# Optimization experiments

Hardware: AMD Instinct MI355X
Metric: run time of the kernel (lower is better)

The kernel has to match this reference:

```python
import jax, jax.numpy as jnp
import numpy as np
from jax import lax

B, C, H, W = 16, 512, 32, 32
CQ = C // 16


def _conv(x, w, b):
    # NCHW input, OIHW kernel, 3x3 stride-1 'SAME' == torch padding=1
    o = lax.conv_general_dilated(x, w, (1, 1), 'SAME',
                                 dimension_numbers=('NCHW', 'OIHW', 'NCHW'))
    return o + b[None, :, None, None]


def setup_inputs() -> dict:
    key = jax.random.key(0)
    ks = jax.random.split(key, 8)
    fan_q = C * 9
    fan_v = C * 9
    return {
        'x': jax.random.normal(ks[0], (B, C, H, W), jnp.float32),
        'y': jax.random.normal(ks[1], (B, C, H, W), jnp.float32),
        'wq': jax.random.normal(ks[2], (CQ, C, 3, 3), jnp.float32) / np.sqrt(fan_q),
        'bq': jnp.zeros((CQ,), jnp.float32),
        'wk': jax.random.normal(ks[3], (CQ, C, 3, 3), jnp.float32) / np.sqrt(fan_q),
        'bk': jnp.zeros((CQ,), jnp.float32),
        'wv': jax.random.normal(ks[4], (C, C, 3, 3), jnp.float32) / np.sqrt(fan_v),
        'bv': jnp.zeros((C,), jnp.float32),
    }


def reference(x, y, wq, bq, wk, bk, wv, bv):
    b, c, h, w = x.shape
    n = h * w
    q = _conv(x, wq, bq).reshape(b, -1, n)   # (B, CQ, N)
    k = _conv(y, wk, bk).reshape(b, -1, n)   # (B, CQ, N)
    v = _conv(y, wv, bv).reshape(b, c, n)    # (B, C, N)
    # energy[b, i, j] = <q[:, i], k[:, j]>  (unscaled, non-causal)
    energy = jnp.einsum('bdi,bdj->bij', q, k)           # (B, N, N)
    attn = jax.nn.softmax(energy, axis=-1)              # softmax over keys j
    # out[b, c, i] = sum_j v[b, c, j] * attn[b, i, j]
    out = jnp.einsum('bcj,bij->bci', v, attn)           # (B, C, N)
    return out.reshape(b, c, h, w)
```

## Files before the change

kernel.cpp:

```cpp
#include <hip/hip_runtime.h>

#define BB 16
#define CCH 512
#define CQD 32
#define HH 32
#define WW 32
#define NN 1024

typedef __attribute__((ext_vector_type(8))) _Float16 half8;
typedef __attribute__((ext_vector_type(4))) _Float16 half4;
typedef __attribute__((ext_vector_type(4))) float f32x4;

static __device__ __forceinline__ void gload_lds16(const void* g, void* l) {
    __builtin_amdgcn_global_load_lds(
        (const __attribute__((address_space(1))) unsigned int*)g,
        (__attribute__((address_space(3))) unsigned int*)l, 16, 0, 0);
}

__global__ __launch_bounds__(256) void prep_img_kernel(
    const float* __restrict__ x, const float* __restrict__ y,
    _Float16* __restrict__ xh, _Float16* __restrict__ yh)
{
    const int h = blockIdx.x, which = blockIdx.y, b = blockIdx.z;
    const float* img = which ? y : x;
    _Float16* imgh   = which ? yh : xh;
    __shared__ float X[64][33];
    const int t = threadIdx.x;
    for (int ci0 = 0; ci0 < CCH; ci0 += 64) {
        __syncthreads();
        #pragma unroll
        for (int i = 0; i < 8; ++i) {
            int ci = i * 8 + (t >> 5), w = t & 31;
            X[ci][w] = img[((size_t)(b * CCH + ci0 + ci) * HH + h) * WW + w];
        }
        __syncthreads();
        int w = t >> 3, g = t & 7;
        half8 o;
        #pragma unroll
        for (int u = 0; u < 8; ++u) o[u] = (_Float16)X[g * 8 + u][w];
        *(half8*)&imgh[(((size_t)b * HH + h) * WW + w) * CCH + ci0 + g * 8] = o;
    }
}

__global__ __launch_bounds__(256) void prep_w_all_kernel(
    const float* __restrict__ wv, const float* __restrict__ wq,
    const float* __restrict__ wk, _Float16* __restrict__ wvh,
    _Float16* __restrict__ wqkh)
{
    const int bid = blockIdx.x;
    const float* src;
    _Float16* dst;
    int co_src, co_dst;
    if (bid < 512)      { src = wv; co_src = bid;       dst = wvh;  co_dst = bid; }
    else if (bid < 544) { src = wq; co_src = bid - 512; dst = wqkh; co_dst = bid - 512; }
    else                { src = wk; co_src = bid - 544; dst = wqkh; co_dst = 32 + (bid - 544); }
    for (int idx = threadIdx.x; idx < 4608; idx += 256) {
        int tap = idx / 512, ci = idx - tap * 512;
        dst[(size_t)co_dst * 4608 + idx] = (_Float16)src[(size_t)co_src * 4608 + ci * 9 + tap];
    }
}

__global__ __launch_bounds__(256, 2) void conv_v_mfma_kernel(
    const _Float16* __restrict__ yh,
    const _Float16* __restrict__ wvh,
    const float* __restrict__ bvb,
    _Float16* __restrict__ vout)
{
    const int pt  = blockIdx.x;
    const int co0 = blockIdx.y * 64;
    const int b   = blockIdx.z;

    __shared__ __align__(16) _Float16 Wl[64 * 296];
    __shared__ __align__(16) _Float16 Yl[10 * 34 * 40];

    const int t    = threadIdx.x;
    const int lane = t & 63;
    const int wv4  = t >> 6;
    const int l15  = lane & 15;
    const int kg   = lane >> 4;

    f32x4 acc[4][4];
    #pragma unroll
    for (int m = 0; m < 4; ++m)
        #pragma unroll
        for (int n = 0; n < 4; ++n) {
            f32x4 z = {0.f, 0.f, 0.f, 0.f};
            acc[m][n] = z;
        }

    const int r0 = pt * 8;
    int bbase[4];
    #pragma unroll
    for (int n = 0; n < 4; ++n) {
        int pxl = wv4 * 64 + n * 16 + l15;
        int rl = pxl >> 5, cl = pxl & 31;
        bbase[n] = (rl * 34 + cl) * 40 + kg * 8;
    }
    int abase[4];
    #pragma unroll
    for (int m = 0; m < 4; ++m)
        abase[m] = (m * 16 + l15) * 296 + kg * 8;

    #pragma unroll 1
    for (int ci0 = 0; ci0 < CCH; ci0 += 32) {
        __syncthreads();
        #pragma unroll
        for (int i = 0; i < 10; ++i) {
            int d = t + i * 256;
            if (d < 2368) {
                int c = d / 37, rem = d - c * 37;
                const _Float16* g = (rem < 36)
                    ? &wvh[(size_t)(co0 + c) * 4608 + (rem >> 2) * 512 + ci0 + (rem & 3) * 8]
                    : wvh;
                gload_lds16(g, (char*)Wl + (size_t)(i * 256 + wv4 * 64) * 16);
            }
        }
        for (int idx = t; idx < 1360; idx += 256) {
            int hw = idx >> 2, part = idx & 3;
            int r = hw / 34, c = hw - r * 34;
            int gh = r0 - 1 + r, gw = c - 1;
            half8 v;
            if (gh >= 0 && gh < HH && gw >= 0 && gw < WW) {
                v = *(const half8*)&yh[(((size_t)b * HH + gh) * WW + gw) * CCH + ci0 + part * 8];
            } else {
                #pragma unroll
                for (int u = 0; u < 8; ++u) v[u] = (_Float16)0.f;
            }
            *(half8*)&Yl[(r * 34 + c) * 40 + part * 8] = v;
        }
        __syncthreads();

        #pragma unroll
        for (int tap = 0; tap < 9; ++tap) {
            const int dh = tap / 3, dw = tap % 3;
            half8 a[4], bf[4];
            #pragma unroll
            for (int m = 0; m < 4; ++m)
                a[m] = *(const half8*)&Wl[abase[m] + tap * 32];
            #pragma unroll
            for (int n = 0; n < 4; ++n)
                bf[n] = *(const half8*)&Yl[bbase[n] + (dh * 34 + dw) * 40];
            #pragma unroll
            for (int m = 0; m < 4; ++m)
                #pragma unroll
                for (int n = 0; n < 4; ++n)
                    acc[m][n] = __builtin_amdgcn_mfma_f32_16x16x32_f16(a[m], bf[n], acc[m][n], 0, 0, 0);
        }
    }

    #pragma unroll
    for (int m = 0; m < 4; ++m) {
        #pragma unroll
        for (int reg = 0; reg < 4; ++reg) {
            int co = co0 + m * 16 + kg * 4 + reg;
            float bias = bvb[co];
            #pragma unroll
            for (int n = 0; n < 4; ++n) {
                int px = pt * 256 + wv4 * 64 + n * 16 + l15;
                vout[((size_t)b * CCH + co) * NN + px] = (_Float16)(acc[m][n][reg] + bias);
            }
        }
    }
}

__global__ __launch_bounds__(256, 4) void conv_qk_split_kernel(
    const _Float16* __restrict__ xh,
    const _Float16* __restrict__ yh,
    const _Float16* __restrict__ wqkh,
    float* __restrict__ pbuf)
{
    const int pt    = blockIdx.x >> 2;
    const int ks    = blockIdx.x & 3;
    const int which = blockIdx.y;
    const int b     = blockIdx.z;
    const _Float16* in = which ? yh : xh;

    __shared__ _Float16 Wl[32 * 296];
    __shared__ _Float16 Xl[6 * 34 * 40];

    const int t    = threadIdx.x;
    const int lane = t & 63;
    const int w    = t >> 6;
    const int l15  = lane & 15;
    const int kg   = lane >> 4;

    f32x4 acc[2][2];
    #pragma unroll
    for (int m = 0; m < 2; ++m)
        #pragma unroll
        for (int n = 0; n < 2; ++n) {
            f32x4 z = {0.f, 0.f, 0.f, 0.f};
            acc[m][n] = z;
        }

    const int r0 = pt * 4;
    int bbase[2];
    #pragma unroll
    for (int n = 0; n < 2; ++n) {
        int pxl = w * 32 + n * 16 + l15;
        int rl = pxl >> 5, cl = pxl & 31;
        bbase[n] = (rl * 34 + cl) * 40 + kg * 8;
    }
    int abase[2];
    #pragma unroll
    for (int m = 0; m < 2; ++m)
        abase[m] = (m * 16 + l15) * 296 + kg * 8;

    #pragma unroll 1
    for (int cc = 0; cc < 4; ++cc) {
        const int ci0 = ks * 128 + cc * 32;
        __syncthreads();
        for (int idx = t; idx < 1152; idx += 256) {
            int c = idx / 36, rem = idx - c * 36;
            int tap = rem >> 2, part = rem & 3;
            half8 v = *(const half8*)&wqkh[(size_t)(which * 32 + c) * 4608 + tap * 512 + ci0 + part * 8];
            *(half8*)&Wl[c * 296 + tap * 32 + part * 8] = v;
        }
        for (int idx = t; idx < 816; idx += 256) {
            int hw = idx >> 2, part = idx & 3;
            int r = hw / 34, c = hw - r * 34;
            int gh = r0 - 1 + r, gw = c - 1;
            half8 v;
            if (gh >= 0 && gh < HH && gw >= 0 && gw < WW) {
                v = *(const half8*)&in[(((size_t)b * HH + gh) * WW + gw) * CCH + ci0 + part * 8];
            } else {
                #pragma unroll
                for (int u = 0; u < 8; ++u) v[u] = (_Float16)0.f;
            }
            *(half8*)&Xl[(r * 34 + c) * 40 + part * 8] = v;
        }
        __syncthreads();

        #pragma unroll
        for (int tap = 0; tap < 9; ++tap) {
            const int dh = tap / 3, dw = tap % 3;
            half8 a[2], bfr[2];
            #pragma unroll
            for (int m = 0; m < 2; ++m)
                a[m] = *(const half8*)&Wl[abase[m] + tap * 32];
            #pragma unroll
            for (int n = 0; n < 2; ++n)
                bfr[n] = *(const half8*)&Xl[bbase[n] + (dh * 34 + dw) * 40];
            #pragma unroll
            for (int m = 0; m < 2; ++m)
                #pragma unroll
                for (int n = 0; n < 2; ++n)
                    acc[m][n] = __builtin_amdgcn_mfma_f32_16x16x32_f16(a[m], bfr[n], acc[m][n], 0, 0, 0);
        }
    }

    float* pb = &pbuf[(((size_t)(ks * 2 + which) * BB + b) * NN) * CQD];
    #pragma unroll
    for (int n = 0; n < 2; ++n) {
        int px = pt * 128 + w * 32 + n * 16 + l15;
        #pragma unroll
        for (int m = 0; m < 2; ++m) {
            float4 o = make_float4(acc[m][n][0], acc[m][n][1], acc[m][n][2], acc[m][n][3]);
            *(float4*)&pb[(size_t)px * CQD + m * 16 + kg * 4] = o;
        }
    }
}

__global__ __launch_bounds__(256) void qk_reduce_kernel(
    const float* __restrict__ pbuf,
    const float* __restrict__ bq, const float* __restrict__ bk,
    _Float16* __restrict__ qh, _Float16* __restrict__ kh)
{
    const int gid   = blockIdx.x * 256 + threadIdx.x;
    const int cog   = gid & 7;
    const int px    = (gid >> 3) & 1023;
    const int b     = (gid >> 13) & 15;
    const int which = gid >> 17;

    const size_t base = (((size_t)which * BB + b) * NN + px) * CQD + cog * 4;
    const size_t kstep = (size_t)2 * BB * NN * CQD;
    float4 s = *(const float4*)&pbuf[base];
    #pragma unroll
    for (int ks = 1; ks < 4; ++ks) {
        float4 p = *(const float4*)&pbuf[base + ks * kstep];
        s.x += p.x; s.y += p.y; s.z += p.z; s.w += p.w;
    }
    const float* bias = which ? bk : bq;
    float4 bv = *(const float4*)&bias[cog * 4];
    half4 o;
    o[0] = (_Float16)(s.x + bv.x);
    o[1] = (_Float16)(s.y + bv.y);
    o[2] = (_Float16)(s.z + bv.z);
    o[3] = (_Float16)(s.w + bv.w);
    _Float16* out = which ? kh : qh;
    *(half4*)&out[((size_t)b * NN + px) * CQD + cog * 4] = o;
}

__global__ __launch_bounds__(256, 2) void attn_fused_kernel(
    const _Float16* __restrict__ qh,
    const _Float16* __restrict__ kh,
    const _Float16* __restrict__ v,
    float* __restrict__ out)
{
    const int wg   = blockIdx.x;
    const int virt = (wg & 7) * 64 + (wg >> 3);
    const int b    = virt >> 5;
    const int i0   = (virt & 31) * 32;

    __shared__ _Float16 Kl[128 * 40];
    __shared__ _Float16 Vl[128 * 136];
    __shared__ _Float16 Pl[32 * 136];
    __shared__ float redm[32][17];
    __shared__ float redl[32][17];

    const int t    = threadIdx.x;
    const int lane = t & 63;
    const int w    = t >> 6;
    const int l15  = lane & 15;
    const int kg   = lane >> 4;

    half8 qb[2];
    #pragma unroll
    for (int n = 0; n < 2; ++n)
        qb[n] = *(const half8*)&qh[((size_t)b * NN + i0 + n * 16 + l15) * CQD + kg * 8];

    float m[2] = {-3.0e38f, -3.0e38f}, l[2] = {0.f, 0.f};
    #pragma unroll 1
    for (int jp = 0; jp < 8; ++jp) {
        __syncthreads();
        #pragma unroll
        for (int r = 0; r < 2; ++r) {
            int idx = t + r * 256;
            int j = idx >> 2, part = idx & 3;
            *(half8*)&Kl[j * 40 + part * 8] =
                *(const half8*)&kh[((size_t)b * NN + jp * 128 + j) * CQD + part * 8];
        }
        __syncthreads();
        #pragma unroll
        for (int ht = 0; ht < 2; ++ht) {
            half8 ak = *(const half8*)&Kl[(ht * 64 + w * 16 + l15) * 40 + kg * 8];
            #pragma unroll
            for (int n = 0; n < 2; ++n) {
                f32x4 s = {0.f, 0.f, 0.f, 0.f};
                s = __builtin_amdgcn_mfma_f32_16x16x32_f16(ak, qb[n], s, 0, 0, 0);
                float tm = fmaxf(fmaxf(s[0], s[1]), fmaxf(s[2], s[3]));
                float m2 = fmaxf(m[n], tm);
                l[n] = l[n] * __expf(m[n] - m2)
                     + __expf(s[0] - m2) + __expf(s[1] - m2)
                     + __expf(s[2] - m2) + __expf(s[3] - m2);
                m[n] = m2;
            }
        }
    }
    __syncthreads();
    #pragma unroll
    for (int n = 0; n < 2; ++n) {
        redm[n * 16 + l15][w * 4 + kg] = m[n];
        redl[n * 16 + l15][w * 4 + kg] = l[n];
    }
    __syncthreads();
    float mr[2], rl[2];
    #pragma unroll
    for (int n = 0; n < 2; ++n) {
        const int i = n * 16 + l15;
        float M = redm[i][0];
        #pragma unroll
        for (int p = 1; p < 16; ++p) M = fmaxf(M, redm[i][p]);
        float L = 0.f;
        #pragma unroll
        for (int p = 0; p < 16; ++p) L += redl[i][p] * __expf(redm[i][p] - M);
        mr[n] = M;
        rl[n] = 1.f / L;
    }

    f32x4 acc[4][2][2];
    #pragma unroll
    for (int cc = 0; cc < 4; ++cc)
        #pragma unroll
        for (int mm = 0; mm < 2; ++mm)
            #pragma unroll
            for (int n = 0; n < 2; ++n) {
                f32x4 z = {0.f, 0.f, 0.f, 0.f};
                acc[cc][mm][n] = z;
            }

    #pragma unroll 1
    for (int jp = 0; jp < 8; ++jp) {
        __syncthreads();
        #pragma unroll
        for (int r = 0; r < 2; ++r) {
            int idx = t + r * 256;
            int j = idx >> 2, part = idx & 3;
            *(half8*)&Kl[j * 40 + part * 8] =
                *(const half8*)&kh[((size_t)b * NN + jp * 128 + j) * CQD + part * 8];
        }
        __syncthreads();
        #pragma unroll
        for (int ht = 0; ht < 2; ++ht) {
            half8 ak = *(const half8*)&Kl[(ht * 64 + w * 16 + l15) * 40 + kg * 8];
            #pragma unroll
            for (int n = 0; n < 2; ++n) {
                f32x4 s = {0.f, 0.f, 0.f, 0.f};
                s = __builtin_amdgcn_mfma_f32_16x16x32_f16(ak, qb[n], s, 0, 0, 0);
                half4 p4;
                #pragma unroll
                for (int reg = 0; reg < 4; ++reg)
                    p4[reg] = (_Float16)(__expf(s[reg] - mr[n]) * rl[n]);
                *(half4*)&Pl[(n * 16 + l15) * 136 + ht * 64 + w * 16 + kg * 4] = p4;
            }
        }
        #pragma unroll
        for (int cc = 0; cc < 4; ++cc) {
            __syncthreads();
            #pragma unroll
            for (int r = 0; r < 8; ++r) {
                int idx = t + r * 256;
                int c = idx >> 4, part = idx & 15;
                *(half8*)&Vl[c * 136 + part * 8] =
                    *(const half8*)&v[((size_t)b * CCH + cc * 128 + c) * NN + jp * 128 + part * 8];
            }
            __syncthreads();
            #pragma unroll
            for (int ks = 0; ks < 4; ++ks) {
                half8 pb[2], va[2];
                #pragma unroll
                for (int n = 0; n < 2; ++n)
                    pb[n] = *(const half8*)&Pl[(n * 16 + l15) * 136 + ks * 32 + kg * 8];
                #pragma unroll
                for (int mm = 0; mm < 2; ++mm)
                    va[mm] = *(const half8*)&Vl[(w * 32 + mm * 16 + l15) * 136 + ks * 32 + kg * 8];
                #pragma unroll
                for (int mm = 0; mm < 2; ++mm)
                    #pragma unroll
                    for (int n = 0; n < 2; ++n)
                        acc[cc][mm][n] = __builtin_amdgcn_mfma_f32_16x16x32_f16(va[mm], pb[n], acc[cc][mm][n], 0, 0, 0);
            }
        }
    }

    #pragma unroll
    for (int cc = 0; cc < 4; ++cc)
        #pragma unroll
        for (int mm = 0; mm < 2; ++mm)
            #pragma unroll
            for (int n = 0; n < 2; ++n)
                #pragma unroll
                for (int reg = 0; reg < 4; ++reg) {
                    int c = cc * 128 + w * 32 + mm * 16 + kg * 4 + reg;
                    out[((size_t)b * CCH + c) * NN + i0 + n * 16 + l15] = acc[cc][mm][n][reg];
                }
}

extern "C" void kernel_launch(void* const* d_in, const int* in_sizes, int n_in,
                              void* d_out, int out_size, void* d_ws, size_t ws_size,
                              hipStream_t stream) {
    const float* x  = (const float*)d_in[0];
    const float* y  = (const float*)d_in[1];
    const float* wq = (const float*)d_in[2];
    const float* bq = (const float*)d_in[3];
    const float* wk = (const float*)d_in[4];
    const float* bk = (const float*)d_in[5];
    const float* wv = (const float*)d_in[6];
    const float* bv = (const float*)d_in[7];
    float* out = (float*)d_out;

    _Float16* qhb = (_Float16*)d_ws;
    _Float16* khb = qhb + (size_t)BB * NN * CQD;
    _Float16* vb   = khb + (size_t)BB * NN * CQD;
    _Float16* yhb  = vb + (size_t)BB * CCH * NN;
    _Float16* xhb  = yhb + (size_t)BB * NN * CCH;
    _Float16* wvh  = xhb + (size_t)BB * NN * CCH;
    _Float16* wqkh = wvh + (size_t)512 * 4608;
    float* pbuf = (float*)vb;

    prep_img_kernel<<<dim3(HH, 2, BB), 256, 0, stream>>>(x, y, xhb, yhb);
    prep_w_all_kernel<<<dim3(576), 256, 0, stream>>>(wv, wq, wk, wvh, wqkh);
    conv_qk_split_kernel<<<dim3(32, 2, BB), 256, 0, stream>>>(xhb, yhb, wqkh, pbuf);
    qk_reduce_kernel<<<dim3(1024), 256, 0, stream>>>(pbuf, bq, bk, qhb, khb);
    conv_v_mfma_kernel<<<dim3(4, 8, BB), 256, 0, stream>>>(yhb, wvh, bv, vb);
    attn_fused_kernel<<<dim3(512), 256, 0, stream>>>(qhb, khb, vb, out);
}
```

Baseline: 181.8 us.

## Pre-pad fp16 images and use direct global-to-LDS loads in conv kernels

The image prep kernel now writes zero-padded 34x34 NHWC fp16 buffers, so the convolution tile loads need no bounds checks. Both the V conv and the QK conv replace register-staged LDS fills with global_load_lds 16-byte async copies, using a 5-slot row stride (40 halves) that matches the existing padded LDS layout. The QK weight tile also switches to direct LDS loads. This removes per-element branching and VGPR round trips in the load phase, at the cost of slightly larger workspace buffers and extra padding writes in the prep kernel.

```diff
diff --git a/kernel.cpp b/kernel.cpp
--- a/kernel.cpp
+++ b/kernel.cpp
@@ -6,6 +6,7 @@
 #define HH 32
 #define WW 32
 #define NN 1024
+#define PH 34
 
 typedef __attribute__((ext_vector_type(8))) _Float16 half8;
 typedef __attribute__((ext_vector_type(4))) _Float16 half4;
@@ -19,26 +20,43 @@
 
 __global__ __launch_bounds__(256) void prep_img_kernel(
     const float* __restrict__ x, const float* __restrict__ y,
-    _Float16* __restrict__ xh, _Float16* __restrict__ yh)
+    _Float16* __restrict__ xp, _Float16* __restrict__ yp)
 {
-    const int h = blockIdx.x, which = blockIdx.y, b = blockIdx.z;
+    const int h = blockIdx.x;
+    const int which = blockIdx.y, b = blockIdx.z;
     const float* img = which ? y : x;
-    _Float16* imgh   = which ? yh : xh;
+    _Float16* row = (which ? yp : xp) + (size_t)(b * PH + h) * PH * CCH;
+    const int t = threadIdx.x;
+    const int gh = h - 1;
+
+    half8 z;
+    #pragma unroll
+    for (int u = 0; u < 8; ++u) z[u] = (_Float16)0.f;
+
+    if (gh < 0 || gh >= HH) {
+        for (int idx = t; idx < PH * CCH / 8; idx += 256)
+            *(half8*)&row[(size_t)idx * 8] = z;
+        return;
+    }
+
     __shared__ float X[64][33];
-    const int t = threadIdx.x;
     for (int ci0 = 0; ci0 < CCH; ci0 += 64) {
         __syncthreads();
         #pragma unroll
         for (int i = 0; i < 8; ++i) {
             int ci = i * 8 + (t >> 5), w = t & 31;
-            X[ci][w] = img[((size_t)(b * CCH + ci0 + ci) * HH + h) * WW + w];
+            X[ci][w] = img[((size_t)(b * CCH + ci0 + ci) * HH + gh) * WW + w];
         }
         __syncthreads();
         int w = t >> 3, g = t & 7;
         half8 o;
         #pragma unroll
         for (int u = 0; u < 8; ++u) o[u] = (_Float16)X[g * 8 + u][w];
-        *(half8*)&imgh[(((size_t)b * HH + h) * WW + w) * CCH + ci0 + g * 8] = o;
+        *(half8*)&row[(size_t)(w + 1) * CCH + ci0 + g * 8] = o;
+        if (t < 16) {
+            int col = (t < 8) ? 0 : 33;
+            *(half8*)&row[(size_t)col * CCH + ci0 + (t & 7) * 8] = z;
+        }
     }
 }
 
@@ -61,7 +79,7 @@
 }
 
 __global__ __launch_bounds__(256, 2) void conv_v_mfma_kernel(
-    const _Float16* __restrict__ yh,
+    const _Float16* __restrict__ yp,
     const _Float16* __restrict__ wvh,
     const float* __restrict__ bvb,
     _Float16* __restrict__ vout)
@@ -71,7 +89,7 @@
     const int b   = blockIdx.z;
 
     __shared__ __align__(16) _Float16 Wl[64 * 296];
-    __shared__ __align__(16) _Float16 Yl[10 * 34 * 40];
+    __shared__ __align__(16) _Float16 Yl[13824];
 
     const int t    = threadIdx.x;
     const int lane = t & 63;
@@ -88,7 +106,7 @@
             acc[m][n] = z;
         }
 
-    const int r0 = pt * 8;
+    const int r0p = pt * 8;
     int bbase[4];
     #pragma unroll
     for (int n = 0; n < 4; ++n) {
@@ -115,18 +133,18 @@
                 gload_lds16(g, (char*)Wl + (size_t)(i * 256 + wv4 * 64) * 16);
             }
         }
-        for (int idx = t; idx < 1360; idx += 256) {
-            int hw = idx >> 2, part = idx & 3;
-            int r = hw / 34, c = hw - r * 34;
-            int gh = r0 - 1 + r, gw = c - 1;
-            half8 v;
-            if (gh >= 0 && gh < HH && gw >= 0 && gw < WW) {
-                v = *(const half8*)&yh[(((size_t)b * HH + gh) * WW + gw) * CCH + ci0 + part * 8];
-            } else {
-                #pragma unroll
-                for (int u = 0; u < 8; ++u) v[u] = (_Float16)0.f;
-            }
-            *(half8*)&Yl[(r * 34 + c) * 40 + part * 8] = v;
+        #pragma unroll
+        for (int i = 0; i < 7; ++i) {
+            int d = t + i * 256;
+            if (d < 1728) {
+                int rc = d / 5, part = d - rc * 5;
+                const _Float16* g = yp;
+                if (rc < 340 && part < 4) {
+                    int r = rc / 34, c = rc - r * 34;
+                    g = &yp[((size_t)(b * PH + r0p + r) * PH + c) * CCH + ci0 + part * 8];
+                }
+                gload_lds16(g, (char*)Yl + (size_t)(i * 256 + wv4 * 64) * 16);
+            }
         }
         __syncthreads();
 
@@ -164,8 +182,8 @@
 }
 
 __global__ __launch_bounds__(256, 4) void conv_qk_split_kernel(
-    const _Float16* __restrict__ xh,
-    const _Float16* __restrict__ yh,
+    const _Float16* __restrict__ xp,
+    const _Float16* __restrict__ yp,
     const _Float16* __restrict__ wqkh,
     float* __restrict__ pbuf)
 {
@@ -173,10 +191,10 @@
     const int ks    = blockIdx.x & 3;
     const int which = blockIdx.y;
     const int b     = blockIdx.z;
-    const _Float16* in = which ? yh : xh;
-
-    __shared__ _Float16 Wl[32 * 296];
-    __shared__ _Float16 Xl[6 * 34 * 40];
+    const _Float16* in = which ? yp : xp;
+
+    __shared__ __align__(16) _Float16 Wl[9728];
+    __shared__ __align__(16) _Float16 Xl[8192];
 
     const int t    = threadIdx.x;
     const int lane = t & 63;
@@ -193,7 +211,7 @@
             acc[m][n] = z;
         }
 
-    const int r0 = pt * 4;
+    const int r0p = pt * 4;
     int bbase[2];
     #pragma unroll
     for (int n = 0; n < 2; ++n) {
@@ -210,24 +228,29 @@
     for (int cc = 0; cc < 4; ++cc) {
         const int ci0 = ks * 128 + cc * 32;
         __syncthreads();
-        for (int idx = t; idx < 1152; idx += 256) {
-            int c = idx / 36, rem = idx - c * 36;
-            int tap = rem >> 2, part = rem & 3;
-            half8 v = *(const half8*)&wqkh[(size_t)(which * 32 + c) * 4608 + tap * 512 + ci0 + part * 8];
-            *(half8*)&Wl[c * 296 + tap * 32 + part * 8] = v;
-        }
-        for (int idx = t; idx < 816; idx += 256) {
-            int hw = idx >> 2, part = idx & 3;
-            int r = hw / 34, c = hw - r * 34;
-            int gh = r0 - 1 + r, gw = c - 1;
-            half8 v;
-            if (gh >= 0 && gh < HH && gw >= 0 && gw < WW) {
-                v = *(const half8*)&in[(((size_t)b * HH + gh) * WW + gw) * CCH + ci0 + part * 8];
-            } else {
-                #pragma unroll
-                for (int u = 0; u < 8; ++u) v[u] = (_Float16)0.f;
-            }
-            *(half8*)&Xl[(r * 34 + c) * 40 + part * 8] = v;
+        #pragma unroll
+        for (int i = 0; i < 5; ++i) {
+            int d = t + i * 256;
+            if (d < 1216) {
+                const _Float16* g = wqkh;
+                if (d < 1184) {
+                    int c = d / 37, rem = d - c * 37;
+                    if (rem < 36)
+                        g = &wqkh[(size_t)(which * 32 + c) * 4608 + (rem >> 2) * 512 + ci0 + (rem & 3) * 8];
+                }
+                gload_lds16(g, (char*)Wl + (size_t)(i * 256 + w * 64) * 16);
+            }
+        }
+        #pragma unroll
+        for (int i = 0; i < 4; ++i) {
+            int d = t + i * 256;
+            int rc = d / 5, part = d - rc * 5;
+            const _Float16* g = in;
+            if (rc < 204 && part < 4) {
+                int r = rc / 34, c = rc - r * 34;
+                g = &in[((size_t)(b * PH + r0p + r) * PH + c) * CCH + ci0 + part * 8];
+            }
+            gload_lds16(g, (char*)Xl + (size_t)(i * 256 + w * 64) * 16);
         }
         __syncthreads();
 
@@ -462,16 +485,16 @@
     _Float16* qhb = (_Float16*)d_ws;
     _Float16* khb = qhb + (size_t)BB * NN * CQD;
     _Float16* vb   = khb + (size_t)BB * NN * CQD;
-    _Float16* yhb  = vb + (size_t)BB * CCH * NN;
-    _Float16* xhb  = yhb + (size_t)BB * NN * CCH;
-    _Float16* wvh  = xhb + (size_t)BB * NN * CCH;
+    _Float16* ypb  = vb + (size_t)BB * CCH * NN;
+    _Float16* xpb  = ypb + (size_t)BB * PH * PH * CCH;
+    _Float16* wvh  = xpb + (size_t)BB * PH * PH * CCH;
     _Float16* wqkh = wvh + (size_t)512 * 4608;
     float* pbuf = (float*)vb;
 
-    prep_img_kernel<<<dim3(HH, 2, BB), 256, 0, stream>>>(x, y, xhb, yhb);
+    prep_img_kernel<<<dim3(PH, 2, BB), 256, 0, stream>>>(x, y, xpb, ypb);
     prep_w_all_kernel<<<dim3(576), 256, 0, stream>>>(wv, wq, wk, wvh, wqkh);
-    conv_qk_split_kernel<<<dim3(32, 2, BB), 256, 0, stream>>>(xhb, yhb, wqkh, pbuf);
+    conv_qk_split_kernel<<<dim3(32, 2, BB), 256, 0, stream>>>(xpb, ypb, wqkh, pbuf);
     qk_reduce_kernel<<<dim3(1024), 256, 0, stream>>>(pbuf, bq, bk, qhb, khb);
-    conv_v_mfma_kernel<<<dim3(4, 8, BB), 256, 0, stream>>>(yhb, wvh, bv, vb);
+    conv_v_mfma_kernel<<<dim3(4, 8, BB), 256, 0, stream>>>(ypb, wvh, bv, vb);
     attn_fused_kernel<<<dim3(512), 256, 0, stream>>>(qhb, khb, vb, out);
 }
```

Result: faster. 173.7 us (-4.4%).
